# Optimization experiments

Measured on AMD Instinct MI355X. Metric: run time of the kernel, lower is better.

Reference implementation:

```python
import jax, jax.numpy as jnp
import numpy as np

B, N, D, H = 8, 1024, 256, 4  # batch, seq, input_dim==output_dim, heads
EPS = 1e-6


def _ln(h, gamma, beta):
    mu = jnp.mean(h, axis=-1, keepdims=True)
    var = jnp.mean(jnp.square(h - mu), axis=-1, keepdims=True)
    return (h - mu) * jax.lax.rsqrt(var + EPS) * gamma + beta


def setup_inputs() -> dict:
    key = jax.random.key(0)
    ks = jax.random.split(key, 8)
    x = jax.random.normal(ks[0], (B, N, D), dtype=jnp.float32)
    mask = jax.random.randint(ks[1], (B, N), 0, 2, dtype=jnp.int32)
    wq = jax.random.normal(ks[2], (H, D, D), dtype=jnp.float32) * 0.05
    wk = jax.random.normal(ks[3], (H, D, D), dtype=jnp.float32) * 0.05
    wv = jax.random.normal(ks[4], (H, D, D), dtype=jnp.float32) * 0.05
    wg = jax.random.uniform(ks[5], (H, D, D), dtype=jnp.float32, minval=-0.05, maxval=0.05)
    out_w = jax.random.normal(ks[6], (D * H, D), dtype=jnp.float32) * 0.05
    out_b = jnp.zeros((D,), dtype=jnp.float32)
    ln_g = jnp.ones((D,), jnp.float32); ln_b = jnp.zeros((D,), jnp.float32)
    lnr_g = jnp.ones((D,), jnp.float32); lnr_b = jnp.zeros((D,), jnp.float32)
    lno_g = jnp.ones((D,), jnp.float32); lno_b = jnp.zeros((D,), jnp.float32)
    return dict(x=x, mask=mask, wq=wq, wk=wk, wv=wv, wg=wg, out_w=out_w, out_b=out_b,
                ln_g=ln_g, ln_b=ln_b, lnr_g=lnr_g, lnr_b=lnr_b, lno_g=lno_g, lno_b=lno_b)


def reference(x, mask, wq, wk, wv, wg, out_w, out_b, ln_g, ln_b, lnr_g, lnr_b, lno_g, lno_b):
    m = mask.astype(jnp.float32)              # (B,N)
    scale = 1.0 / jnp.sqrt(jnp.float32(D))
    x_norm = _ln(x, ln_g, ln_b)               # (B,N,D)
    q = jnp.einsum('bnd,hde->hbne', x_norm, wq)
    k = jnp.einsum('bmd,hde->hbme', x_norm, wk)
    v = jnp.einsum('bmd,hde->hbme', x_norm, wv)
    att = jnp.einsum('hbne,hbme->hbnm', q, k) * scale  # (H,B,N,N)
    amask = m[:, :, None] * m[:, None, :]              # (B,N,N) outer-product mask
    att = att + (1.0 - amask)[None] * (-1e9)           # additive mask
    att = jax.nn.softmax(att, axis=-1) * amask[None]   # multiplicative mask
    out = jnp.einsum('hbnm,hbme->hbne', att, v)        # (H,B,N,D)
    gate = jax.nn.sigmoid(jnp.einsum('bnd,hde->hbne', x_norm, wg))
    out = out * gate
    out = out + x[None]                                # resnet per head
    out = _ln(out, lnr_g, lnr_b)
    out = jnp.transpose(out, (1, 2, 3, 0)).reshape(x.shape[0], x.shape[1], D * H)
    out = out @ out_w + out_b                          # (B,N,D)
    out = out + x                                      # resnet
    out = _ln(out, lno_g, lno_b)
    out = out * m[..., None]
    return out
```

## Files before the change

kernel.cpp:

```cpp
#include <hip/hip_runtime.h>
#include <hip/hip_bf16.h>

#define Bb 8
#define Nn 1024
#define Dd 256
#define Hh 4
#define ROWS 8192
#define EPSf 1e-6f

typedef __bf16 bf16t;
typedef bf16t bf16x8 __attribute__((ext_vector_type(8)));
typedef float f32x4 __attribute__((ext_vector_type(4)));

#define MFMA(a, b, c) __builtin_amdgcn_mfma_f32_16x16x32_bf16((a), (b), (c), 0, 0, 0)
#define GLB_U32(p) ((const __attribute__((address_space(1))) unsigned int*)(p))
#define LDS_U32(p) ((__attribute__((address_space(3))) unsigned int*)(p))

__device__ __forceinline__ bf16x8 load8(const bf16t* p) { return *(const bf16x8*)p; }

__device__ __forceinline__ float ldin(const void* p, size_t i, int flag) {
  return flag ? (float)((const bf16t*)p)[i] : ((const float*)p)[i];
}

__global__ __launch_bounds__(256) void k_prepall(
    const void* __restrict__ x,
    const void* __restrict__ wq, const void* __restrict__ wk,
    const void* __restrict__ wv, const void* __restrict__ wg,
    const void* __restrict__ ow,
    const void* __restrict__ lng, const void* __restrict__ lnb,
    const void* __restrict__ lnrg, const void* __restrict__ lnrb,
    const void* __restrict__ lnog, const void* __restrict__ lnob,
    const void* __restrict__ ob,
    bf16t* __restrict__ xn, float* __restrict__ xf, bf16t* __restrict__ wtAll,
    bf16t* __restrict__ owT, float* __restrict__ pf, int* __restrict__ flagOut) {
  __shared__ int sflag;
  {
    if (threadIdx.x < 64) {
      int lane = threadIdx.x;
      int cnt = 0;
      const unsigned int* xw = (const unsigned int*)x;
#pragma unroll
      for (int i = 0; i < 4; ++i) {
        unsigned int b1 = (xw[lane * 4 + i] >> 8) & 0x7F;
        if (b1 >= 0x3B && b1 <= 0x43) cnt++;
      }
#pragma unroll
      for (int off = 32; off > 0; off >>= 1) cnt += __shfl_xor(cnt, off);
      if (lane == 0) sflag = (cnt > 128) ? 1 : 0;
    }
    __syncthreads();
  }
  const int flag = sflag;
  const int bid = blockIdx.x;

  if (bid < 2048) {
    int row = bid * 4 + (threadIdx.x >> 6);
    int lane = threadIdx.x & 63;
    size_t base = (size_t)row * Dd;
    float v[4]; float s = 0.f, s2 = 0.f;
#pragma unroll
    for (int i = 0; i < 4; ++i) {
      v[i] = ldin(x, base + lane * 4 + i, flag);
      s += v[i]; s2 += v[i] * v[i];
    }
#pragma unroll
    for (int off = 32; off > 0; off >>= 1) {
      s += __shfl_xor(s, off);
      s2 += __shfl_xor(s2, off);
    }
    float mu = s * (1.f / Dd);
    float var = fmaxf(s2 * (1.f / Dd) - mu * mu, 0.f);
    float rs = rsqrtf(var + EPSf);
#pragma unroll
    for (int i = 0; i < 4; ++i) {
      int d = lane * 4 + i;
      xf[base + d] = v[i];
      xn[base + d] = (bf16t)((v[i] - mu) * rs * ldin(lng, d, flag) + ldin(lnb, d, flag));
    }
  } else if (bid < 3328) {
    __shared__ bf16t tile[32][33];
    int t = bid - 2048;
    const void* in; bf16t* out; int R, C; size_t ibase;
    int r0, c0;
    if (t < 1024) {
      int w = t >> 8, z = (t >> 6) & 3, t64 = t & 63;
      r0 = (t64 >> 3) * 32; c0 = (t64 & 7) * 32;
      const void* srcs[4] = {wq, wk, wv, wg};
      const int tslot[4] = {0, 1, 3, 2};
      in = srcs[w]; ibase = (size_t)z * 65536;
      out = wtAll + (size_t)(tslot[w] * 4 + z) * 65536;
      R = 256; C = 256;
    } else {
      int t2 = t - 1024;
      c0 = (t2 & 7) * 32; r0 = (t2 >> 3) * 32;
      in = ow; ibase = 0; out = owT; R = 1024; C = 256;
    }
    int tx = threadIdx.x & 31, ty = threadIdx.x >> 5;
#pragma unroll
    for (int i = 0; i < 32; i += 8)
      tile[ty + i][tx] = (bf16t)ldin(in, ibase + (size_t)(r0 + ty + i) * C + c0 + tx, flag);
    __syncthreads();
#pragma unroll
    for (int i = 0; i < 32; i += 8)
      out[(size_t)(c0 + ty + i) * R + r0 + tx] = tile[tx][ty + i];
  } else {
    const void* ps[7] = {lng, lnb, lnrg, lnrb, lnog, lnob, ob};
#pragma unroll
    for (int j = 0; j < 7; ++j)
      pf[j * 256 + threadIdx.x] = ldin(ps[j], threadIdx.x, flag);
    if (threadIdx.x == 0) *flagOut = flag;
  }
}

__global__ __launch_bounds__(256) void k_qkvg(
    const bf16t* __restrict__ xn, const bf16t* __restrict__ wtAll,
    bf16t* __restrict__ q, bf16t* __restrict__ kk,
    bf16t* __restrict__ g, bf16t* __restrict__ vt) {
  const int wave = threadIdx.x >> 6, lane = threadIdx.x & 63;
  const int quad = lane >> 4, l16 = lane & 15;
  const int mi = blockIdx.x, ni = blockIdx.y;
  const int row0 = mi * 128;
  const int instw = ni >> 1, colIn = (ni & 1) * 128;
  const int tt = instw >> 2, h = instw & 3;
  const int rB = (wave >> 1) * 64, cB = (wave & 1) * 64;

  const bf16t* Bsrc = wtAll + (size_t)instw * 65536 + (size_t)colIn * 256;

  __shared__ bf16t aT[4096];
  __shared__ bf16t bT[4096];
  __shared__ bf16t ct[128 * 136];

  f32x4 acc[4][4];
#pragma unroll
  for (int i = 0; i < 4; ++i)
#pragma unroll
    for (int j = 0; j < 4; ++j) acc[i][j] = (f32x4){0.f, 0.f, 0.f, 0.f};

  for (int k0 = 0; k0 < 256; k0 += 32) {
#pragma unroll
    for (int ii = 0; ii < 2; ++ii) {
      int inst = wave * 2 + ii;
      int idx = inst * 64 + lane;
      int r = idx >> 2, cp = idx & 3;
      int c = cp ^ ((r >> 1) & 3);
      __builtin_amdgcn_global_load_lds(GLB_U32(xn + (size_t)(row0 + r) * 256 + k0 + c * 8),
                                       LDS_U32(aT + inst * 512), 16, 0, 0);
    }
#pragma unroll
    for (int ii = 0; ii < 2; ++ii) {
      int inst = wave * 2 + ii;
      int idx = inst * 64 + lane;
      int r = idx >> 2, cp = idx & 3;
      int c = cp ^ ((r >> 1) & 3);
      __builtin_amdgcn_global_load_lds(GLB_U32(Bsrc + (size_t)r * 256 + k0 + c * 8),
                                       LDS_U32(bT + inst * 512), 16, 0, 0);
    }
    __syncthreads();

    bf16x8 aF[4], bF[4];
#pragma unroll
    for (int i = 0; i < 4; ++i) {
      int r = rB + i * 16 + l16;
      aF[i] = *(const bf16x8*)&aT[(r * 4 + (quad ^ ((r >> 1) & 3))) * 8];
    }
#pragma unroll
    for (int j = 0; j < 4; ++j) {
      int r = cB + j * 16 + l16;
      bF[j] = *(const bf16x8*)&bT[(r * 4 + (quad ^ ((r >> 1) & 3))) * 8];
    }
#pragma unroll
    for (int i = 0; i < 4; ++i)
#pragma unroll
      for (int j = 0; j < 4; ++j)
        acc[i][j] = MFMA(aF[i], bF[j], acc[i][j]);
    __syncthreads();
  }

  const bool tr = (tt == 3);
#pragma unroll
  for (int i = 0; i < 4; ++i)
#pragma unroll
    for (int j = 0; j < 4; ++j)
#pragma unroll
      for (int r = 0; r < 4; ++r) {
        int rl = rB + i * 16 + quad * 4 + r, cl = cB + j * 16 + l16;
        if (tr) ct[cl * 136 + rl] = (bf16t)acc[i][j][r];
        else    ct[rl * 136 + cl] = (bf16t)acc[i][j][r];
      }
  __syncthreads();
  if (!tr) {
    bf16t* base = (tt == 0 ? q : (tt == 1 ? kk : g)) +
                  (size_t)h * ROWS * Dd + (size_t)row0 * Dd + colIn;
#pragma unroll
    for (int it = 0; it < 8; ++it) {
      int rl = it * 16 + (threadIdx.x >> 4), c8 = (threadIdx.x & 15) * 8;
      *(bf16x8*)(base + (size_t)rl * Dd + c8) = *(const bf16x8*)&ct[rl * 136 + c8];
    }
  } else {
    int bb = row0 >> 10, n0 = row0 & 1023;
    bf16t* base = vt + (size_t)(h * Bb + bb) * Dd * Nn + (size_t)colIn * Nn + n0;
#pragma unroll
    for (int it = 0; it < 8; ++it) {
      int el = it * 16 + (threadIdx.x >> 4), c8 = (threadIdx.x & 15) * 8;
      *(bf16x8*)(base + (size_t)el * Nn + c8) = *(const bf16x8*)&ct[el * 136 + c8];
    }
  }
}

__global__ __launch_bounds__(256) void k_flash(
    const bf16t* __restrict__ qb, const bf16t* __restrict__ kb,
    const bf16t* __restrict__ vtb, const bf16t* __restrict__ gb,
    const float* __restrict__ xf, const int* __restrict__ mask,
    const float* __restrict__ pf, bf16t* __restrict__ tout) {
  const int wave = threadIdx.x >> 6, lane = threadIdx.x & 63;
  const int quad = lane >> 4, l16 = lane & 15;
  const int lin = blockIdx.x + 16 * blockIdx.y + 128 * blockIdx.z;
  const int hbp = lin & 31, tile = lin >> 5;
  const int b = hbp & 7, h = hbp >> 3;
  const int qrow0 = tile * 64 + wave * 16;

  const bf16t* Q = qb + (size_t)hbp * Nn * Dd;
  const bf16t* K = kb + (size_t)hbp * Nn * Dd;
  const bf16t* V = vtb + (size_t)hbp * Dd * Nn;
  const bf16t* G = gb + (size_t)hbp * Nn * Dd;

  __shared__ bf16t klds[32 * 256];
  __shared__ bf16t vlds[2][256 * 32];
  __shared__ bf16t pl[4 * 16 * 32];
  __shared__ unsigned char cmu[Nn];

#define SWZ(row_) (((row_) & 3) ^ (((row_) >> 2) & 3))
#define STAGE_K(kt_) do {                                                      \
    _Pragma("unroll") for (int i_ = 0; i_ < 4; ++i_) {                         \
      int inst_ = wave * 4 + i_; int qq_ = inst_ * 64 + lane;                  \
      int r_ = qq_ >> 5, cp_ = qq_ & 31; int c_ = cp_ ^ (r_ & 15);             \
      __builtin_amdgcn_global_load_lds(                                        \
          GLB_U32(K + (size_t)((kt_) + r_) * Dd + c_ * 8),                     \
          LDS_U32(klds + inst_ * 512), 16, 0, 0); } } while (0)
#define STAGE_V(kt_, buf_) do {                                                \
    _Pragma("unroll") for (int i_ = 0; i_ < 4; ++i_) {                         \
      int inst_ = wave * 4 + i_; int qq_ = inst_ * 64 + lane;                  \
      int r_ = qq_ >> 2, cp_ = qq_ & 3; int c_ = cp_ ^ SWZ(r_);                \
      __builtin_amdgcn_global_load_lds(                                        \
          GLB_U32(V + (size_t)r_ * Nn + (kt_) + c_ * 8),                       \
          LDS_U32(vlds[buf_] + inst_ * 512), 16, 0, 0); } } while (0)

  STAGE_V(0, 0);
  STAGE_K(0);
  for (int i = threadIdx.x; i < Nn; i += 256) cmu[i] = (unsigned char)mask[b * Nn + i];

  bf16x8 aq[8];
#pragma unroll
  for (int k8 = 0; k8 < 8; ++k8)
    aq[k8] = load8(Q + (size_t)(qrow0 + l16) * Dd + k8 * 32 + quad * 8);

  f32x4 oacc[16];
#pragma unroll
  for (int j = 0; j < 16; ++j) oacc[j] = (f32x4){0.f, 0.f, 0.f, 0.f};
  float lpart[4] = {0.f, 0.f, 0.f, 0.f};

  const float scale = 0.0625f;

  for (int kt = 0; kt < Nn; kt += 32) {
    const int vcur = (kt >> 5) & 1;
    __syncthreads();
    if (kt + 32 < Nn) STAGE_V(kt + 32, vcur ^ 1);

    f32x4 sacc[2];
    sacc[0] = (f32x4){0.f, 0.f, 0.f, 0.f};
    sacc[1] = (f32x4){0.f, 0.f, 0.f, 0.f};
#pragma unroll
    for (int k8 = 0; k8 < 8; ++k8)
#pragma unroll
      for (int j = 0; j < 2; ++j) {
        bf16x8 bk = *(const bf16x8*)&klds[((j * 16 + l16) * 32 + ((k8 * 4 + quad) ^ l16)) * 8];
        sacc[j] = MFMA(aq[k8], bk, sacc[j]);
      }

    int cmv0 = cmu[kt + l16], cmv1 = cmu[kt + 16 + l16];
#pragma unroll
    for (int j = 0; j < 2; ++j) {
      int cmv = j ? cmv1 : cmv0;
#pragma unroll
      for (int r = 0; r < 4; ++r) {
        float e = (cmv != 0) ? __expf(sacc[j][r] * scale) : 0.f;
        lpart[r] += e;
        int prow = quad * 4 + r;
        pl[wave * 512 + (prow * 4 + ((j * 2 + (l16 >> 3)) ^ SWZ(prow))) * 8 + (l16 & 7)] = (bf16t)e;
      }
    }

    __builtin_amdgcn_s_barrier();
    if (kt + 32 < Nn) STAGE_K(kt + 32);

    bf16x8 ap = *(const bf16x8*)&pl[wave * 512 + (l16 * 4 + (quad ^ SWZ(l16))) * 8];
#pragma unroll
    for (int j = 0; j < 16; ++j) {
      int e = j * 16 + l16;
      bf16x8 bv = *(const bf16x8*)&vlds[vcur][(e * 4 + (quad ^ SWZ(e))) * 8];
      oacc[j] = MFMA(ap, bv, oacc[j]);
    }
  }

#pragma unroll
  for (int r = 0; r < 4; ++r)
#pragma unroll
    for (int off = 1; off < 16; off <<= 1)
      lpart[r] += __shfl_xor(lpart[r], off);

  float inv[4];
#pragma unroll
  for (int r = 0; r < 4; ++r) {
    int rmv = cmu[qrow0 + quad * 4 + r];
    inv[r] = (rmv != 0 && lpart[r] > 1e-20f) ? 1.f / lpart[r] : 0.f;
  }
  float ps[4] = {0.f, 0.f, 0.f, 0.f}, pq[4] = {0.f, 0.f, 0.f, 0.f};
#pragma unroll
  for (int j = 0; j < 16; ++j) {
    int e = j * 16 + l16;
#pragma unroll
    for (int r = 0; r < 4; ++r) {
      int n = qrow0 + quad * 4 + r;
      float gv = (float)G[(size_t)n * Dd + e];
      float xv = xf[(size_t)(b * Nn + n) * Dd + e];
      float o = oacc[j][r] * inv[r] * (1.f / (1.f + __expf(-gv))) + xv;
      oacc[j][r] = o;
      ps[r] += o; pq[r] += o * o;
    }
  }
#pragma unroll
  for (int r = 0; r < 4; ++r) {
#pragma unroll
    for (int off = 1; off < 16; off <<= 1) {
      ps[r] += __shfl_xor(ps[r], off);
      pq[r] += __shfl_xor(pq[r], off);
    }
    float mu = ps[r] * (1.f / Dd);
    float rs = rsqrtf(fmaxf(pq[r] * (1.f / Dd) - mu * mu, 0.f) + EPSf);
    ps[r] = mu; pq[r] = rs;
  }
#pragma unroll
  for (int j = 0; j < 16; ++j) {
    int e = j * 16 + l16;
    float lg = pf[2 * 256 + e], lb = pf[3 * 256 + e];
#pragma unroll
    for (int r = 0; r < 4; ++r) {
      int n = qrow0 + quad * 4 + r;
      tout[((size_t)(b * Nn + n) * Dd + e) * Hh + h] =
          (bf16t)((oacc[j][r] - ps[r]) * pq[r] * lg + lb);
    }
  }
#undef STAGE_K
#undef STAGE_V
#undef SWZ
}

__global__ __launch_bounds__(256) void k_out(
    const bf16t* __restrict__ t, const bf16t* __restrict__ owT,
    const float* __restrict__ xf, const int* __restrict__ mask,
    const float* __restrict__ pf, void* __restrict__ outp,
    const int* __restrict__ flagp) {
  const int flag = *flagp;
  const int wave = threadIdx.x >> 6, lane = threadIdx.x & 63;
  const int quad = lane >> 4, l16 = lane & 15;
  const int row0 = blockIdx.x * 16;

  __shared__ bf16t aT[512];
  __shared__ bf16t bT[8192];
  __shared__ float redS[4][16], redQ[4][16];

  f32x4 acc[4];
#pragma unroll
  for (int j = 0; j < 4; ++j) acc[j] = (f32x4){0.f, 0.f, 0.f, 0.f};

  for (int k0 = 0; k0 < 1024; k0 += 32) {
    if (wave == 0) {
      int r = lane >> 2, cp = lane & 3;
      int c = cp ^ ((r >> 1) & 3);
      __builtin_amdgcn_global_load_lds(GLB_U32(t + (size_t)(row0 + r) * 1024 + k0 + c * 8),
                                       LDS_U32(aT), 16, 0, 0);
    }
#pragma unroll
    for (int ii = 0; ii < 4; ++ii) {
      int inst = wave * 4 + ii;
      int idx = inst * 64 + lane;
      int r = idx >> 2, cp = idx & 3;
      int c = cp ^ ((r >> 1) & 3);
      __builtin_amdgcn_global_load_lds(GLB_U32(owT + (size_t)r * 1024 + k0 + c * 8),
                                       LDS_U32(bT + inst * 512), 16, 0, 0);
    }
    __syncthreads();
    bf16x8 a = *(const bf16x8*)&aT[(l16 * 4 + (quad ^ ((l16 >> 1) & 3))) * 8];
#pragma unroll
    for (int j = 0; j < 4; ++j) {
      int r = wave * 64 + j * 16 + l16;
      bf16x8 bb = *(const bf16x8*)&bT[(r * 4 + (quad ^ ((r >> 1) & 3))) * 8];
      acc[j] = MFMA(a, bb, acc[j]);
    }
    __syncthreads();
  }

  float ps[4] = {0.f, 0.f, 0.f, 0.f}, pq[4] = {0.f, 0.f, 0.f, 0.f};
#pragma unroll
  for (int j = 0; j < 4; ++j) {
    int e = wave * 64 + j * 16 + l16;
    float bias = pf[6 * 256 + e];
#pragma unroll
    for (int r = 0; r < 4; ++r) {
      int rr = row0 + quad * 4 + r;
      float o = acc[j][r] + bias + xf[(size_t)rr * Dd + e];
      acc[j][r] = o;
      ps[r] += o; pq[r] += o * o;
    }
  }
#pragma unroll
  for (int r = 0; r < 4; ++r) {
#pragma unroll
    for (int off = 1; off < 16; off <<= 1) {
      ps[r] += __shfl_xor(ps[r], off);
      pq[r] += __shfl_xor(pq[r], off);
    }
    if (l16 == 0) { redS[wave][quad * 4 + r] = ps[r]; redQ[wave][quad * 4 + r] = pq[r]; }
  }
  __syncthreads();
  float mu[4], rs[4], mk[4];
#pragma unroll
  for (int r = 0; r < 4; ++r) {
    int rl = quad * 4 + r;
    float ts = redS[0][rl] + redS[1][rl] + redS[2][rl] + redS[3][rl];
    float tq = redQ[0][rl] + redQ[1][rl] + redQ[2][rl] + redQ[3][rl];
    float m_ = ts * (1.f / Dd);
    mu[r] = m_;
    rs[r] = rsqrtf(fmaxf(tq * (1.f / Dd) - m_ * m_, 0.f) + EPSf);
    mk[r] = (float)mask[row0 + rl];
  }
#pragma unroll
  for (int j = 0; j < 4; ++j) {
    int e = wave * 64 + j * 16 + l16;
    float lg = pf[4 * 256 + e], lb = pf[5 * 256 + e];
#pragma unroll
    for (int r = 0; r < 4; ++r) {
      int rr = row0 + quad * 4 + r;
      float o = ((acc[j][r] - mu[r]) * rs[r] * lg + lb) * mk[r];
      size_t idx = (size_t)rr * Dd + e;
      if (flag) ((bf16t*)outp)[idx] = (bf16t)o;
      else      ((float*)outp)[idx] = o;
    }
  }
}

extern "C" void kernel_launch(void* const* d_in, const int* in_sizes, int n_in,
                              void* d_out, int out_size, void* d_ws, size_t ws_size,
                              hipStream_t stream) {
  const void* x    = d_in[0];
  const int*  mask = (const int*)d_in[1];
  const void* wq   = d_in[2];
  const void* wk   = d_in[3];
  const void* wv   = d_in[4];
  const void* wg   = d_in[5];
  const void* ow   = d_in[6];
  const void* ob   = d_in[7];
  const void* lng  = d_in[8];
  const void* lnb  = d_in[9];
  const void* lnrg = d_in[10];
  const void* lnrb = d_in[11];
  const void* lnog = d_in[12];
  const void* lnob = d_in[13];

  char* w = (char*)d_ws;
  int*   flag  = (int*)w;
  float* pf    = (float*)(w + 256);
  w += 8192;
  float* xf    = (float*)w; w += (size_t)ROWS * Dd * 4;
  bf16t* xn    = (bf16t*)w; w += (size_t)ROWS * Dd * 2;
  bf16t* wtAll = (bf16t*)w; w += (size_t)16 * Dd * Dd * 2;
  bf16t* owT   = (bf16t*)w; w += (size_t)Dd * 1024 * 2;
  bf16t* tb    = (bf16t*)w; w += (size_t)ROWS * 1024 * 2;
  bf16t* qb    = (bf16t*)w; w += (size_t)Hh * ROWS * Dd * 2;
  bf16t* kb    = (bf16t*)w; w += (size_t)Hh * ROWS * Dd * 2;
  bf16t* gb    = (bf16t*)w; w += (size_t)Hh * ROWS * Dd * 2;
  bf16t* vtb   = (bf16t*)w; w += (size_t)Hh * ROWS * Dd * 2;

  dim3 blk(256);
  k_prepall<<<dim3(3329), blk, 0, stream>>>(x, wq, wk, wv, wg, ow,
                                            lng, lnb, lnrg, lnrb, lnog, lnob, ob,
                                            xn, xf, wtAll, owT, pf, flag);
  k_qkvg<<<dim3(64, 32), blk, 0, stream>>>(xn, wtAll, qb, kb, gb, vtb);
  k_flash<<<dim3(16, 8, 4), blk, 0, stream>>>(qb, kb, vtb, gb, xf, mask, pf, tb);
  k_out<<<dim3(512), blk, 0, stream>>>(tb, owT, xf, mask, pf, d_out, flag);
}
```

Measured before the change: 213.8 us.

## Split PV accumulation across waves by output columns with 4x4 register tiling

In the flash kernel, the P·V stage now has each wave compute a 64-row by 64-column output tile covering all four waves' P rows, instead of 16 rows by all 256 columns. Each wave reads 4 P fragments and 4 V fragments per step, fewer than the 16 V fragment loads per wave before, which cuts LDS read traffic. In exchange, the row-sum normalizer and the LayerNorm statistics must now be combined across waves through shared memory, which adds two block barriers and an lgkmcnt wait before the existing barrier.

```diff
diff --git a/kernel.cpp b/kernel.cpp
--- a/kernel.cpp
+++ b/kernel.cpp
@@ -217,7 +217,8 @@
   const int lin = blockIdx.x + 16 * blockIdx.y + 128 * blockIdx.z;
   const int hbp = lin & 31, tile = lin >> 5;
   const int b = hbp & 7, h = hbp >> 3;
-  const int qrow0 = tile * 64 + wave * 16;
+  const int row0 = tile * 64;
+  const int qrow0 = row0 + wave * 16;
 
   const bf16t* Q = qb + (size_t)hbp * Nn * Dd;
   const bf16t* K = kb + (size_t)hbp * Nn * Dd;
@@ -228,6 +229,8 @@
   __shared__ bf16t vlds[2][256 * 32];
   __shared__ bf16t pl[4 * 16 * 32];
   __shared__ unsigned char cmu[Nn];
+  __shared__ float lshare[64];
+  __shared__ float redS[4][64], redQ[4][64];
 
 #define SWZ(row_) (((row_) & 3) ^ (((row_) >> 2) & 3))
 #define STAGE_K(kt_) do {                                                      \
@@ -254,9 +257,11 @@
   for (int k8 = 0; k8 < 8; ++k8)
     aq[k8] = load8(Q + (size_t)(qrow0 + l16) * Dd + k8 * 32 + quad * 8);
 
-  f32x4 oacc[16];
-#pragma unroll
-  for (int j = 0; j < 16; ++j) oacc[j] = (f32x4){0.f, 0.f, 0.f, 0.f};
+  f32x4 oacc[4][4];
+#pragma unroll
+  for (int m = 0; m < 4; ++m)
+#pragma unroll
+    for (int n = 0; n < 4; ++n) oacc[m][n] = (f32x4){0.f, 0.f, 0.f, 0.f};
   float lpart[4] = {0.f, 0.f, 0.f, 0.f};
 
   const float scale = 0.0625f;
@@ -290,16 +295,24 @@
       }
     }
 
+    __asm__ volatile("s_waitcnt lgkmcnt(0)" ::: "memory");
     __builtin_amdgcn_s_barrier();
     if (kt + 32 < Nn) STAGE_K(kt + 32);
 
-    bf16x8 ap = *(const bf16x8*)&pl[wave * 512 + (l16 * 4 + (quad ^ SWZ(l16))) * 8];
-#pragma unroll
-    for (int j = 0; j < 16; ++j) {
-      int e = j * 16 + l16;
-      bf16x8 bv = *(const bf16x8*)&vlds[vcur][(e * 4 + (quad ^ SWZ(e))) * 8];
-      oacc[j] = MFMA(ap, bv, oacc[j]);
-    }
+    bf16x8 ap[4], bv[4];
+#pragma unroll
+    for (int m = 0; m < 4; ++m)
+      ap[m] = *(const bf16x8*)&pl[m * 512 + (l16 * 4 + (quad ^ SWZ(l16))) * 8];
+#pragma unroll
+    for (int n = 0; n < 4; ++n) {
+      int e = wave * 64 + n * 16 + l16;
+      bv[n] = *(const bf16x8*)&vlds[vcur][(e * 4 + (quad ^ SWZ(e))) * 8];
+    }
+#pragma unroll
+    for (int m = 0; m < 4; ++m)
+#pragma unroll
+      for (int n = 0; n < 4; ++n)
+        oacc[m][n] = MFMA(ap[m], bv[n], oacc[m][n]);
   }
 
 #pragma unroll
@@ -307,49 +320,84 @@
 #pragma unroll
     for (int off = 1; off < 16; off <<= 1)
       lpart[r] += __shfl_xor(lpart[r], off);
-
-  float inv[4];
-#pragma unroll
-  for (int r = 0; r < 4; ++r) {
-    int rmv = cmu[qrow0 + quad * 4 + r];
-    inv[r] = (rmv != 0 && lpart[r] > 1e-20f) ? 1.f / lpart[r] : 0.f;
-  }
-  float ps[4] = {0.f, 0.f, 0.f, 0.f}, pq[4] = {0.f, 0.f, 0.f, 0.f};
-#pragma unroll
-  for (int j = 0; j < 16; ++j) {
-    int e = j * 16 + l16;
+  if (l16 == 0) {
+#pragma unroll
+    for (int r = 0; r < 4; ++r) lshare[wave * 16 + quad * 4 + r] = lpart[r];
+  }
+  __syncthreads();
+
+  float inv[4][4];
+#pragma unroll
+  for (int m = 0; m < 4; ++m)
 #pragma unroll
     for (int r = 0; r < 4; ++r) {
-      int n = qrow0 + quad * 4 + r;
-      float gv = (float)G[(size_t)n * Dd + e];
-      float xv = xf[(size_t)(b * Nn + n) * Dd + e];
-      float o = oacc[j][r] * inv[r] * (1.f / (1.f + __expf(-gv))) + xv;
-      oacc[j][r] = o;
-      ps[r] += o; pq[r] += o * o;
-    }
-  }
-#pragma unroll
-  for (int r = 0; r < 4; ++r) {
-#pragma unroll
-    for (int off = 1; off < 16; off <<= 1) {
-      ps[r] += __shfl_xor(ps[r], off);
-      pq[r] += __shfl_xor(pq[r], off);
-    }
-    float mu = ps[r] * (1.f / Dd);
-    float rs = rsqrtf(fmaxf(pq[r] * (1.f / Dd) - mu * mu, 0.f) + EPSf);
-    ps[r] = mu; pq[r] = rs;
-  }
-#pragma unroll
-  for (int j = 0; j < 16; ++j) {
-    int e = j * 16 + l16;
-    float lg = pf[2 * 256 + e], lb = pf[3 * 256 + e];
+      int rl = m * 16 + quad * 4 + r;
+      float lv = lshare[rl];
+      int rmv = cmu[row0 + rl];
+      inv[m][r] = (rmv != 0 && lv > 1e-20f) ? 1.f / lv : 0.f;
+    }
+
+  float ps[4][4], pq[4][4];
+#pragma unroll
+  for (int m = 0; m < 4; ++m)
+#pragma unroll
+    for (int r = 0; r < 4; ++r) { ps[m][r] = 0.f; pq[m][r] = 0.f; }
+#pragma unroll
+  for (int m = 0; m < 4; ++m)
+#pragma unroll
+    for (int n = 0; n < 4; ++n) {
+      int e = wave * 64 + n * 16 + l16;
+#pragma unroll
+      for (int r = 0; r < 4; ++r) {
+        int ng = row0 + m * 16 + quad * 4 + r;
+        float gv = (float)G[(size_t)ng * Dd + e];
+        float xv = xf[(size_t)(b * Nn + ng) * Dd + e];
+        float o = oacc[m][n][r] * inv[m][r] * (1.f / (1.f + __expf(-gv))) + xv;
+        oacc[m][n][r] = o;
+        ps[m][r] += o; pq[m][r] += o * o;
+      }
+    }
+#pragma unroll
+  for (int m = 0; m < 4; ++m)
 #pragma unroll
     for (int r = 0; r < 4; ++r) {
-      int n = qrow0 + quad * 4 + r;
-      tout[((size_t)(b * Nn + n) * Dd + e) * Hh + h] =
-          (bf16t)((oacc[j][r] - ps[r]) * pq[r] * lg + lb);
-    }
-  }
+#pragma unroll
+      for (int off = 1; off < 16; off <<= 1) {
+        ps[m][r] += __shfl_xor(ps[m][r], off);
+        pq[m][r] += __shfl_xor(pq[m][r], off);
+      }
+      if (l16 == 0) {
+        redS[wave][m * 16 + quad * 4 + r] = ps[m][r];
+        redQ[wave][m * 16 + quad * 4 + r] = pq[m][r];
+      }
+    }
+  __syncthreads();
+
+  float mu[4][4], rsv[4][4];
+#pragma unroll
+  for (int m = 0; m < 4; ++m)
+#pragma unroll
+    for (int r = 0; r < 4; ++r) {
+      int rl = m * 16 + quad * 4 + r;
+      float ts = redS[0][rl] + redS[1][rl] + redS[2][rl] + redS[3][rl];
+      float tq = redQ[0][rl] + redQ[1][rl] + redQ[2][rl] + redQ[3][rl];
+      float m_ = ts * (1.f / Dd);
+      mu[m][r] = m_;
+      rsv[m][r] = rsqrtf(fmaxf(tq * (1.f / Dd) - m_ * m_, 0.f) + EPSf);
+    }
+#pragma unroll
+  for (int m = 0; m < 4; ++m)
+#pragma unroll
+    for (int n = 0; n < 4; ++n) {
+      int e = wave * 64 + n * 16 + l16;
+      float lg = pf[2 * 256 + e], lb = pf[3 * 256 + e];
+#pragma unroll
+      for (int r = 0; r < 4; ++r) {
+        int ng = row0 + m * 16 + quad * 4 + r;
+        tout[((size_t)(b * Nn + ng) * Dd + e) * Hh + h] =
+            (bf16t)((oacc[m][n][r] - mu[m][r]) * rsv[m][r] * lg + lb);
+      }
+    }
 #undef STAGE_K
 #undef STAGE_V
 #undef SWZ
```

New measurement: 256.7 us. +20.1%, slower.
